# Kernel tuning notes

Measured on AMD Instinct MI355X. Metric: run time of the kernel, lower is better.

Reference implementation:

```python
import jax, jax.numpy as jnp
import numpy as np

NB_CLASSES = 100000
SZ_EMBED = 64
SZ_BATCH = 1024


def setup_inputs() -> dict:
    key = jax.random.key(0)
    k1, k2, k3 = jax.random.split(key, 3)
    xs = jax.random.normal(k1, (SZ_BATCH, SZ_EMBED), dtype=jnp.float32)
    ys = jax.random.randint(k2, (SZ_BATCH,), 0, NB_CLASSES, dtype=jnp.int64)
    # xavier_uniform for an Embedding(nb_classes, sz_embed)
    limit = float(np.sqrt(6.0 / (NB_CLASSES + SZ_EMBED)))
    proxies = jax.random.uniform(k3, (NB_CLASSES, SZ_EMBED), dtype=jnp.float32,
                                 minval=-limit, maxval=limit)
    return {"xs": xs, "ys": ys, "proxies": proxies}


def reference(xs, ys, proxies):
    # L2-normalize each proxy row (torch F.normalize; eps guard like torch's 1e-12).
    # Note: the original normalizes the positive proxy with dim=0 on a 1-D vector,
    # which is identical to per-row normalization.
    norms = jnp.linalg.norm(proxies, axis=1, keepdims=True)
    P = proxies / jnp.maximum(norms, 1e-12)                      # [C, D]

    # Squared euclidean distance matrix D[i, c] = ||x_i - P_c||^2 via GEMM
    x_sq = jnp.sum(xs * xs, axis=1, keepdims=True)               # [B, 1]
    p_sq = jnp.sum(P * P, axis=1)                                # [C]
    dist = jnp.maximum(x_sq + p_sq[None, :] - 2.0 * (xs @ P.T), 0.0)  # [B, C]

    logits = -dist                                               # [B, C]
    ys = ys.astype(jnp.int32)
    d_pos = jnp.take_along_axis(dist, ys[:, None], axis=1)[:, 0]  # [B]

    # log sum over negatives (c != y) of exp(-dist)
    neg_mask = jnp.arange(NB_CLASSES)[None, :] != ys[:, None]    # [B, C]
    neg_logits = jnp.where(neg_mask, logits, -jnp.inf)
    log_n = jax.nn.logsumexp(neg_logits, axis=1)                 # [B]

    # -log(p / n) = dist_pos + log(sum_neg exp(-dist))
    per_sample = d_pos + log_n
    return jnp.mean(per_sample)
```

## Files before the change

### kernel.cpp

```cpp
#include <hip/hip_runtime.h>
#include <math.h>

#define B 1024
#define C 100000
#define D 64
#define MT 128
#define TC 256
#define NCH 391
#define NPADROWS (NCH * TC)
#define CPAD (NPADROWS - C)
#define PPR (NCH * 4)
#define L2E 1.4426950408889634f

typedef __attribute__((ext_vector_type(8))) short short8;
typedef __attribute__((ext_vector_type(4))) float f32x4;

#define WS_PART 0
#define WS_CW2  ((size_t)B * PPR * 4)
#define WS_XBF  (WS_CW2 + B * 4)
#define WS_PBF  (WS_XBF + (size_t)B * D * 2)

#define GLB(p) ((const __attribute__((address_space(1))) void*)(p))
#define LDS(p) ((__attribute__((address_space(3))) void*)(p))

static __device__ __forceinline__ unsigned short f2bf(float f) {
    unsigned u = __float_as_uint(f);
    return (unsigned short)((u + 0x7fffu + ((u >> 16) & 1u)) >> 16);
}
static __device__ __forceinline__ float bf_round(float f) {
    return __uint_as_float(((unsigned)f2bf(f)) << 16);
}
static __device__ __forceinline__ float fexp2(float x) {
#if __has_builtin(__builtin_amdgcn_exp2f)
    return __builtin_amdgcn_exp2f(x);
#else
    return __expf(x * 0.6931471805599453f);
#endif
}

__global__ __launch_bounds__(256) void proxynca_prep(
    const float* __restrict__ xs, const float* __restrict__ proxies,
    unsigned short* __restrict__ Xbf, unsigned short* __restrict__ Pbf,
    float* __restrict__ cw2)
{
    const int t = threadIdx.x;
    const int rl = t >> 4, f4 = t & 15;
    const int bb = blockIdx.x;
    if (bb < NPADROWS / 16) {
        int gr = bb * 16 + rl;
        float4 v = make_float4(0.f, 0.f, 0.f, 0.f);
        if (gr < C) v = *(const float4*)(proxies + (size_t)gr * D + f4 * 4);
        float ss = v.x*v.x + v.y*v.y + v.z*v.z + v.w*v.w;
        ss += __shfl_xor(ss, 1); ss += __shfl_xor(ss, 2);
        ss += __shfl_xor(ss, 4); ss += __shfl_xor(ss, 8);
        float rn = 1.0f / fmaxf(sqrtf(ss), 1e-12f);
        ushort4 w;
        w.x = f2bf(v.x * rn); w.y = f2bf(v.y * rn);
        w.z = f2bf(v.z * rn); w.w = f2bf(v.w * rn);
        *(ushort4*)(Pbf + (size_t)gr * D + f4 * 4) = w;
    } else {
        int row = (bb - NPADROWS / 16) * 16 + rl;
        float4 v = *(const float4*)(xs + (size_t)row * D + f4 * 4);
        float ss = v.x*v.x + v.y*v.y + v.z*v.z + v.w*v.w;
        ss += __shfl_xor(ss, 1); ss += __shfl_xor(ss, 2);
        ss += __shfl_xor(ss, 4); ss += __shfl_xor(ss, 8);
        ushort4 w;
        w.x = f2bf(v.x); w.y = f2bf(v.y); w.z = f2bf(v.z); w.w = f2bf(v.w);
        *(ushort4*)(Xbf + (size_t)row * D + f4 * 4) = w;
        if (f4 == 0) cw2[row] = -2.0f * sqrtf(ss) * L2E;
    }
}

__global__ __launch_bounds__(512, 4) void proxynca_main(
    const unsigned short* __restrict__ Xbf, const unsigned short* __restrict__ Pbf,
    const float* __restrict__ cw2v, float* __restrict__ partial)
{
    __shared__ __align__(16) unsigned short Ash[MT * 64];
    __shared__ __align__(16) unsigned short Bsh[TC * 64];
    __shared__ float crow[MT];

    const int t = threadIdx.x;
    const int lane = t & 63;
    const int wv = t >> 6;
    const int row0 = blockIdx.x * MT;
    const int ct = blockIdx.y;

    const unsigned short* Asrc = Xbf + (size_t)row0 * D;
    const unsigned short* Bsrc = Pbf + (size_t)ct * TC * D;

    #pragma unroll
    for (int j = 0; j < 2; ++j) {
        int c = (j * 8 + wv) * 64 + lane;
        int row = c >> 3, q = c & 7;
        int sc = (row << 3) | (q ^ (row & 7));
        __builtin_amdgcn_global_load_lds(GLB(Asrc + sc * 8),
            LDS(Ash + (size_t)(j * 8 + wv) * 512), 16, 0, 0);
    }
    #pragma unroll
    for (int j = 0; j < 4; ++j) {
        int c = (j * 8 + wv) * 64 + lane;
        int row = c >> 3, q = c & 7;
        int sc = (row << 3) | (q ^ (row & 7));
        __builtin_amdgcn_global_load_lds(GLB(Bsrc + sc * 8),
            LDS(Bsh + (size_t)(j * 8 + wv) * 512), 16, 0, 0);
    }
    if (t < MT) crow[t] = cw2v[row0 + t];
    __syncthreads();

    const int quad = lane >> 4, sixt = lane & 15;
    const int mg = wv >> 2, ng = wv & 3;

    short8 af[4][2];
    #pragma unroll
    for (int ms = 0; ms < 4; ++ms) {
        int rowL = mg * 64 + ms * 16 + sixt;
        int sw = rowL & 7;
        af[ms][0] = *(const short8*)(Ash + (size_t)(((rowL << 3) | (quad ^ sw)) * 8));
        af[ms][1] = *(const short8*)(Ash + (size_t)(((rowL << 3) | ((4 + quad) ^ sw)) * 8));
    }
    float cw[4][4];
    #pragma unroll
    for (int ms = 0; ms < 4; ++ms)
        #pragma unroll
        for (int rg = 0; rg < 4; ++rg)
            cw[ms][rg] = crow[mg * 64 + ms * 16 + quad * 4 + rg];

    float s_acc[4][4];
    #pragma unroll
    for (int ms = 0; ms < 4; ++ms)
        #pragma unroll
        for (int rg = 0; rg < 4; ++rg) s_acc[ms][rg] = 0.f;

    #pragma unroll
    for (int ns = 0; ns < 4; ++ns) {
        int classL = ng * 64 + ns * 16 + sixt;
        int sw = classL & 7;
        short8 b0 = *(const short8*)(Bsh + (size_t)(((classL << 3) | (quad ^ sw)) * 8));
        short8 b1 = *(const short8*)(Bsh + (size_t)(((classL << 3) | ((4 + quad) ^ sw)) * 8));
        #pragma unroll
        for (int ms = 0; ms < 4; ++ms) {
            f32x4 acc = {0.f, 0.f, 0.f, 0.f};
            acc = __builtin_amdgcn_mfma_f32_16x16x32_bf16(af[ms][0], b0, acc, 0, 0, 0);
            acc = __builtin_amdgcn_mfma_f32_16x16x32_bf16(af[ms][1], b1, acc, 0, 0, 0);
            #pragma unroll
            for (int rg = 0; rg < 4; ++rg)
                s_acc[ms][rg] += fexp2(fmaf(2.0f * L2E, acc[rg], cw[ms][rg]));
        }
    }

    #pragma unroll
    for (int ms = 0; ms < 4; ++ms)
        #pragma unroll
        for (int rg = 0; rg < 4; ++rg) {
            float s = s_acc[ms][rg];
            s += __shfl_xor(s, 1); s += __shfl_xor(s, 2);
            s += __shfl_xor(s, 4); s += __shfl_xor(s, 8);
            s_acc[ms][rg] = s;
        }
    if (sixt == 0) {
        #pragma unroll
        for (int ms = 0; ms < 4; ++ms)
            #pragma unroll
            for (int rg = 0; rg < 4; ++rg) {
                int row = row0 + mg * 64 + ms * 16 + quad * 4 + rg;
                partial[(size_t)row * PPR + ct * 4 + ng] = s_acc[ms][rg];
            }
    }
}

__global__ __launch_bounds__(256) void proxynca_reduce(
    const float* __restrict__ xs, const int* __restrict__ ys,
    const float* __restrict__ proxies, const float* __restrict__ partial,
    float* __restrict__ out)
{
    __shared__ float acc4[4];
    const int lane = threadIdx.x & 63;
    const int w = threadIdx.x >> 6;
    const int row = blockIdx.x * 4 + w;

    float x = xs[(size_t)row * D + lane];
    int y = ys[row];
    float p = proxies[(size_t)y * D + lane];

    float xx = x * x, pp = p * p;
    #pragma unroll
    for (int off = 1; off < 64; off <<= 1) {
        xx += __shfl_xor(xx, off);
        pp += __shfl_xor(pp, off);
    }
    float nx = sqrtf(xx);
    float rn = 1.0f / fmaxf(sqrtf(pp), 1e-12f);
    float ph = p * rn;

    float xp = x * ph;
    float xpb = bf_round(x) * bf_round(ph);
    #pragma unroll
    for (int off = 1; off < 64; off <<= 1) {
        xp  += __shfl_xor(xp, off);
        xpb += __shfl_xor(xpb, off);
    }

    float s = 0.f;
    for (int j = lane; j < PPR; j += 64) s += partial[(size_t)row * PPR + j];
    #pragma unroll
    for (int off = 1; off < 64; off <<= 1) s += __shfl_xor(s, off);

    if (lane == 0) {
        float cw2r = -2.0f * nx * L2E;
        float e_pos = fexp2(fmaf(2.0f * L2E, xpb, cw2r));
        float e_pad = fexp2(cw2r);
        float s_neg = s - e_pos - (float)CPAD * e_pad;
        acc4[w] = 2.0f * (nx - xp) + logf(s_neg);
    }
    __syncthreads();
    if (threadIdx.x == 0) {
        float v = acc4[0] + acc4[1] + acc4[2] + acc4[3];
        atomicAdd(out, v * (1.0f / (float)B));
    }
}

extern "C" void kernel_launch(void* const* d_in, const int* in_sizes, int n_in,
                              void* d_out, int out_size, void* d_ws, size_t ws_size,
                              hipStream_t stream)
{
    const float* xs      = (const float*)d_in[0];
    const int*   ys      = (const int*)d_in[1];
    const float* proxies = (const float*)d_in[2];
    char* ws = (char*)d_ws;
    float* partial = (float*)(ws + WS_PART);
    float* cw2     = (float*)(ws + WS_CW2);
    unsigned short* Xbf = (unsigned short*)(ws + WS_XBF);
    unsigned short* Pbf = (unsigned short*)(ws + WS_PBF);
    float* out = (float*)d_out;

    hipMemsetAsync(out, 0, sizeof(float), stream);
    proxynca_prep<<<NPADROWS / 16 + B / 16, 256, 0, stream>>>(xs, proxies, Xbf, Pbf, cw2);
    dim3 gridA(B / MT, NCH);
    proxynca_main<<<gridA, 512, 0, stream>>>(Xbf, Pbf, cw2, partial);
    proxynca_reduce<<<B / 4, 256, 0, stream>>>(xs, ys, proxies, partial, out);
}
```

Before: 122.3 us.

## Fuse proxy normalization into main kernel and loop over row tiles per block

Proxy L2 normalization and bf16 conversion move into the main GEMM kernel, so the normalized proxy matrix no longer makes a round trip through global memory. Each block now keeps its 256-class B tile in registers and walks four 128-row X tiles, double-buffering the X tiles into LDS with async loads. Per-wave partial sums are combined in shared memory before being written, which shrinks the partial array fourfold. In exchange the grid drops to 2x391 blocks, which lowers parallelism, and each block now runs a serial loop with two barriers per step.

After: 152.5 us. 1.25x slower.

```diff
diff --git a/kernel.cpp b/kernel.cpp
--- a/kernel.cpp
+++ b/kernel.cpp
@@ -4,21 +4,19 @@
 #define B 1024
 #define C 100000
 #define D 64
-#define MT 128
 #define TC 256
 #define NCH 391
 #define NPADROWS (NCH * TC)
 #define CPAD (NPADROWS - C)
-#define PPR (NCH * 4)
+#define NP NCH
 #define L2E 1.4426950408889634f
 
 typedef __attribute__((ext_vector_type(8))) short short8;
 typedef __attribute__((ext_vector_type(4))) float f32x4;
 
 #define WS_PART 0
-#define WS_CW2  ((size_t)B * PPR * 4)
+#define WS_CW2  ((size_t)B * NP * 4)
 #define WS_XBF  (WS_CW2 + B * 4)
-#define WS_PBF  (WS_XBF + (size_t)B * D * 2)
 
 #define GLB(p) ((const __attribute__((address_space(1))) void*)(p))
 #define LDS(p) ((__attribute__((address_space(3))) void*)(p))
@@ -38,18 +36,57 @@
 #endif
 }
 
-__global__ __launch_bounds__(256) void proxynca_prep(
-    const float* __restrict__ xs, const float* __restrict__ proxies,
-    unsigned short* __restrict__ Xbf, unsigned short* __restrict__ Pbf,
+__global__ __launch_bounds__(256) void proxynca_prepx(
+    const float* __restrict__ xs, unsigned short* __restrict__ Xbf,
     float* __restrict__ cw2)
 {
     const int t = threadIdx.x;
     const int rl = t >> 4, f4 = t & 15;
-    const int bb = blockIdx.x;
-    if (bb < NPADROWS / 16) {
-        int gr = bb * 16 + rl;
+    const int row = blockIdx.x * 16 + rl;
+    const float4 v = *(const float4*)(xs + (size_t)row * D + f4 * 4);
+    float ss = v.x*v.x + v.y*v.y + v.z*v.z + v.w*v.w;
+    ss += __shfl_xor(ss, 1); ss += __shfl_xor(ss, 2);
+    ss += __shfl_xor(ss, 4); ss += __shfl_xor(ss, 8);
+    ushort4 w;
+    w.x = f2bf(v.x); w.y = f2bf(v.y); w.z = f2bf(v.z); w.w = f2bf(v.w);
+    *(ushort4*)(Xbf + (size_t)row * D + f4 * 4) = w;
+    if (f4 == 0) cw2[row] = -2.0f * sqrtf(ss) * L2E;
+}
+
+__global__ __launch_bounds__(512, 4) void proxynca_main(
+    const float* __restrict__ proxies, const unsigned short* __restrict__ Xbf,
+    const float* __restrict__ cw2v, float* __restrict__ partial)
+{
+    __shared__ __align__(16) unsigned short Bsh[TC * 64];
+    __shared__ __align__(16) unsigned short Ash[2][128 * 64];
+    __shared__ float crow[512];
+    __shared__ __align__(16) float scratch[128][4];
+
+    const int t = threadIdx.x;
+    const int lane = t & 63;
+    const int wv = t >> 6;
+    const int rh = blockIdx.x;
+    const int ct = blockIdx.y;
+    const int rbase = rh * 512;
+
+    const unsigned short* Asrc = Xbf + (size_t)rbase * D;
+
+    #pragma unroll
+    for (int j = 0; j < 2; ++j) {
+        int c = (j * 8 + wv) * 64 + lane;
+        int row = c >> 3, q = c & 7;
+        int sc = (row << 3) | (q ^ (row & 7));
+        __builtin_amdgcn_global_load_lds(GLB(Asrc + sc * 8),
+            LDS(&Ash[0][(j * 8 + wv) * 512]), 16, 0, 0);
+    }
+
+    #pragma unroll
+    for (int i = 0; i < 8; ++i) {
+        int idx = i * 512 + t;
+        int r = idx >> 4, f4 = idx & 15;
+        int gc = ct * TC + r;
         float4 v = make_float4(0.f, 0.f, 0.f, 0.f);
-        if (gr < C) v = *(const float4*)(proxies + (size_t)gr * D + f4 * 4);
+        if (gc < C) v = *(const float4*)(proxies + (size_t)gc * D + f4 * 4);
         float ss = v.x*v.x + v.y*v.y + v.z*v.z + v.w*v.w;
         ss += __shfl_xor(ss, 1); ss += __shfl_xor(ss, 2);
         ss += __shfl_xor(ss, 4); ss += __shfl_xor(ss, 8);
@@ -57,114 +94,88 @@
         ushort4 w;
         w.x = f2bf(v.x * rn); w.y = f2bf(v.y * rn);
         w.z = f2bf(v.z * rn); w.w = f2bf(v.w * rn);
-        *(ushort4*)(Pbf + (size_t)gr * D + f4 * 4) = w;
-    } else {
-        int row = (bb - NPADROWS / 16) * 16 + rl;
-        float4 v = *(const float4*)(xs + (size_t)row * D + f4 * 4);
-        float ss = v.x*v.x + v.y*v.y + v.z*v.z + v.w*v.w;
-        ss += __shfl_xor(ss, 1); ss += __shfl_xor(ss, 2);
-        ss += __shfl_xor(ss, 4); ss += __shfl_xor(ss, 8);
-        ushort4 w;
-        w.x = f2bf(v.x); w.y = f2bf(v.y); w.z = f2bf(v.z); w.w = f2bf(v.w);
-        *(ushort4*)(Xbf + (size_t)row * D + f4 * 4) = w;
-        if (f4 == 0) cw2[row] = -2.0f * sqrtf(ss) * L2E;
-    }
-}
-
-__global__ __launch_bounds__(512, 4) void proxynca_main(
-    const unsigned short* __restrict__ Xbf, const unsigned short* __restrict__ Pbf,
-    const float* __restrict__ cw2v, float* __restrict__ partial)
-{
-    __shared__ __align__(16) unsigned short Ash[MT * 64];
-    __shared__ __align__(16) unsigned short Bsh[TC * 64];
-    __shared__ float crow[MT];
-
-    const int t = threadIdx.x;
-    const int lane = t & 63;
-    const int wv = t >> 6;
-    const int row0 = blockIdx.x * MT;
-    const int ct = blockIdx.y;
-
-    const unsigned short* Asrc = Xbf + (size_t)row0 * D;
-    const unsigned short* Bsrc = Pbf + (size_t)ct * TC * D;
-
-    #pragma unroll
-    for (int j = 0; j < 2; ++j) {
-        int c = (j * 8 + wv) * 64 + lane;
-        int row = c >> 3, q = c & 7;
-        int sc = (row << 3) | (q ^ (row & 7));
-        __builtin_amdgcn_global_load_lds(GLB(Asrc + sc * 8),
-            LDS(Ash + (size_t)(j * 8 + wv) * 512), 16, 0, 0);
-    }
-    #pragma unroll
-    for (int j = 0; j < 4; ++j) {
-        int c = (j * 8 + wv) * 64 + lane;
-        int row = c >> 3, q = c & 7;
-        int sc = (row << 3) | (q ^ (row & 7));
-        __builtin_amdgcn_global_load_lds(GLB(Bsrc + sc * 8),
-            LDS(Bsh + (size_t)(j * 8 + wv) * 512), 16, 0, 0);
-    }
-    if (t < MT) crow[t] = cw2v[row0 + t];
+        int q = f4 >> 1, h = f4 & 1;
+        int p = q ^ (r & 7);
+        *(ushort4*)(Bsh + (size_t)((r * 8 + p) * 8 + h * 4)) = w;
+    }
+    crow[t] = cw2v[rbase + t];
     __syncthreads();
 
     const int quad = lane >> 4, sixt = lane & 15;
     const int mg = wv >> 2, ng = wv & 3;
 
-    short8 af[4][2];
-    #pragma unroll
-    for (int ms = 0; ms < 4; ++ms) {
-        int rowL = mg * 64 + ms * 16 + sixt;
-        int sw = rowL & 7;
-        af[ms][0] = *(const short8*)(Ash + (size_t)(((rowL << 3) | (quad ^ sw)) * 8));
-        af[ms][1] = *(const short8*)(Ash + (size_t)(((rowL << 3) | ((4 + quad) ^ sw)) * 8));
-    }
-    float cw[4][4];
-    #pragma unroll
-    for (int ms = 0; ms < 4; ++ms)
-        #pragma unroll
-        for (int rg = 0; rg < 4; ++rg)
-            cw[ms][rg] = crow[mg * 64 + ms * 16 + quad * 4 + rg];
-
-    float s_acc[4][4];
-    #pragma unroll
-    for (int ms = 0; ms < 4; ++ms)
-        #pragma unroll
-        for (int rg = 0; rg < 4; ++rg) s_acc[ms][rg] = 0.f;
-
+    short8 bfr[4][2];
     #pragma unroll
     for (int ns = 0; ns < 4; ++ns) {
-        int classL = ng * 64 + ns * 16 + sixt;
-        int sw = classL & 7;
-        short8 b0 = *(const short8*)(Bsh + (size_t)(((classL << 3) | (quad ^ sw)) * 8));
-        short8 b1 = *(const short8*)(Bsh + (size_t)(((classL << 3) | ((4 + quad) ^ sw)) * 8));
+        int cl = ng * 64 + ns * 16 + sixt;
+        int sw = cl & 7;
+        bfr[ns][0] = *(const short8*)(Bsh + (size_t)(((cl << 3) | (quad ^ sw)) * 8));
+        bfr[ns][1] = *(const short8*)(Bsh + (size_t)(((cl << 3) | ((4 + quad) ^ sw)) * 8));
+    }
+
+    for (int rt = 0; rt < 4; ++rt) {
+        if (rt < 3) {
+            const unsigned short* An = Asrc + (size_t)(rt + 1) * 128 * D;
+            #pragma unroll
+            for (int j = 0; j < 2; ++j) {
+                int c = (j * 8 + wv) * 64 + lane;
+                int row = c >> 3, q = c & 7;
+                int sc = (row << 3) | (q ^ (row & 7));
+                __builtin_amdgcn_global_load_lds(GLB(An + sc * 8),
+                    LDS(&Ash[(rt + 1) & 1][(j * 8 + wv) * 512]), 16, 0, 0);
+            }
+        }
+
+        const unsigned short* Ab = Ash[rt & 1];
+        short8 af[4][2];
         #pragma unroll
         for (int ms = 0; ms < 4; ++ms) {
-            f32x4 acc = {0.f, 0.f, 0.f, 0.f};
-            acc = __builtin_amdgcn_mfma_f32_16x16x32_bf16(af[ms][0], b0, acc, 0, 0, 0);
-            acc = __builtin_amdgcn_mfma_f32_16x16x32_bf16(af[ms][1], b1, acc, 0, 0, 0);
+            int rowL = mg * 64 + ms * 16 + sixt;
+            int sw = rowL & 7;
+            af[ms][0] = *(const short8*)(Ab + (size_t)(((rowL << 3) | (quad ^ sw)) * 8));
+            af[ms][1] = *(const short8*)(Ab + (size_t)(((rowL << 3) | ((4 + quad) ^ sw)) * 8));
+        }
+        float cw[4][4];
+        #pragma unroll
+        for (int ms = 0; ms < 4; ++ms)
             #pragma unroll
             for (int rg = 0; rg < 4; ++rg)
-                s_acc[ms][rg] += fexp2(fmaf(2.0f * L2E, acc[rg], cw[ms][rg]));
+                cw[ms][rg] = crow[rt * 128 + mg * 64 + ms * 16 + quad * 4 + rg];
+
+        float s_acc[4][4];
+        #pragma unroll
+        for (int ms = 0; ms < 4; ++ms)
+            #pragma unroll
+            for (int rg = 0; rg < 4; ++rg) s_acc[ms][rg] = 0.f;
+
+        #pragma unroll
+        for (int ns = 0; ns < 4; ++ns)
+            #pragma unroll
+            for (int ms = 0; ms < 4; ++ms) {
+                f32x4 acc = {0.f, 0.f, 0.f, 0.f};
+                acc = __builtin_amdgcn_mfma_f32_16x16x32_bf16(af[ms][0], bfr[ns][0], acc, 0, 0, 0);
+                acc = __builtin_amdgcn_mfma_f32_16x16x32_bf16(af[ms][1], bfr[ns][1], acc, 0, 0, 0);
+                #pragma unroll
+                for (int rg = 0; rg < 4; ++rg)
+                    s_acc[ms][rg] += fexp2(fmaf(2.0f * L2E, acc[rg], cw[ms][rg]));
+            }
+
+        #pragma unroll
+        for (int ms = 0; ms < 4; ++ms)
+            #pragma unroll
+            for (int rg = 0; rg < 4; ++rg) {
+                float s = s_acc[ms][rg];
+                s += __shfl_xor(s, 1); s += __shfl_xor(s, 2);
+                s += __shfl_xor(s, 4); s += __shfl_xor(s, 8);
+                if (sixt == 0)
+                    scratch[mg * 64 + ms * 16 + quad * 4 + rg][ng] = s;
+            }
+        __syncthreads();
+        if (t < 128) {
+            float4 s4 = *(const float4*)scratch[t];
+            partial[(size_t)(rbase + rt * 128 + t) * NP + ct] = s4.x + s4.y + s4.z + s4.w;
         }
-    }
-
-    #pragma unroll
-    for (int ms = 0; ms < 4; ++ms)
-        #pragma unroll
-        for (int rg = 0; rg < 4; ++rg) {
-            float s = s_acc[ms][rg];
-            s += __shfl_xor(s, 1); s += __shfl_xor(s, 2);
-            s += __shfl_xor(s, 4); s += __shfl_xor(s, 8);
-            s_acc[ms][rg] = s;
-        }
-    if (sixt == 0) {
-        #pragma unroll
-        for (int ms = 0; ms < 4; ++ms)
-            #pragma unroll
-            for (int rg = 0; rg < 4; ++rg) {
-                int row = row0 + mg * 64 + ms * 16 + quad * 4 + rg;
-                partial[(size_t)row * PPR + ct * 4 + ng] = s_acc[ms][rg];
-            }
+        __syncthreads();
     }
 }
 
@@ -201,7 +212,7 @@
     }
 
     float s = 0.f;
-    for (int j = lane; j < PPR; j += 64) s += partial[(size_t)row * PPR + j];
+    for (int j = lane; j < NP; j += 64) s += partial[(size_t)row * NP + j];
     #pragma unroll
     for (int off = 1; off < 64; off <<= 1) s += __shfl_xor(s, off);
 
@@ -230,12 +241,11 @@
     float* partial = (float*)(ws + WS_PART);
     float* cw2     = (float*)(ws + WS_CW2);
     unsigned short* Xbf = (unsigned short*)(ws + WS_XBF);
-    unsigned short* Pbf = (unsigned short*)(ws + WS_PBF);
     float* out = (float*)d_out;
 
     hipMemsetAsync(out, 0, sizeof(float), stream);
-    proxynca_prep<<<NPADROWS / 16 + B / 16, 256, 0, stream>>>(xs, proxies, Xbf, Pbf, cw2);
-    dim3 gridA(B / MT, NCH);
-    proxynca_main<<<gridA, 512, 0, stream>>>(Xbf, Pbf, cw2, partial);
+    proxynca_prepx<<<B / 16, 256, 0, stream>>>(xs, Xbf, cw2);
+    dim3 gridA(2, NCH);
+    proxynca_main<<<gridA, 512, 0, stream>>>(proxies, Xbf, cw2, partial);
     proxynca_reduce<<<B / 4, 256, 0, stream>>>(xs, ys, proxies, partial, out);
 }
```
